# Kernel optimization log

Measured on AMD Instinct MI355X. Metric: run time of the kernel, lower is better.

Reference implementation:

```python
import jax, jax.numpy as jnp
import numpy as np

N = 256  # n_neurons
S = 32   # state_dim
M = 32   # message_dim
E = 32   # edge_dim
B = 64   # batch
N_IN = 16

def setup_inputs() -> dict:
    key = jax.random.key(0)
    ks = jax.random.split(key, 12)
    sc = 0.1
    return {
        "inputs": jax.random.normal(ks[0], (B, N_IN, S), jnp.float32),
        "initial_state": jax.random.normal(ks[1], (N, S), jnp.float32) * sc,
        "edge_matrix": jax.random.normal(ks[2], (N, N, E), jnp.float32) * sc,
        "Wf": jax.random.normal(ks[3], (E, M * S), jnp.float32) * sc,
        "bf": jnp.zeros((M * S,), jnp.float32),
        "Wz": jax.random.normal(ks[4], (M, S), jnp.float32) * sc,
        "Uz": jax.random.normal(ks[5], (S, S), jnp.float32) * sc,
        "bz": jnp.zeros((S,), jnp.float32),
        "Wr": jax.random.normal(ks[6], (M, S), jnp.float32) * sc,
        "Ur": jax.random.normal(ks[7], (S, S), jnp.float32) * sc,
        "br": jnp.zeros((S,), jnp.float32),
        "Wh": jax.random.normal(ks[8], (M, S), jnp.float32) * sc,
        "Uh": jax.random.normal(ks[9], (S, S), jnp.float32) * sc,
        "bh": jnp.zeros((S,), jnp.float32),
        "n_outputs": 16,
    }

def reference(inputs, initial_state, edge_matrix, Wf, bf, Wz, Uz, bz, Wr, Ur, br, Wh, Uh, bh, n_outputs):
    b, n_in, s = inputs.shape
    n = initial_state.shape[0]
    # filter generation: [N,N,E] -> [N,N,M,S]
    filters = (edge_matrix @ Wf + bf).reshape(n, n, M, s)
    # init + scatter inputs into hidden state (neuron i <- inputs[:, i, :])
    h = jnp.tile(initial_state[None], (b, 1, 1)).at[:, :n_in, :].set(inputs)
    # dense edge-filtered message passing: messages[b,j,m] = sum_i filters[i,j,m,s] h[b,i,s]
    messages = jnp.einsum('bis,ijms->bjm', h, filters)
    # GRU update with message as input
    z = jax.nn.sigmoid(messages @ Wz + h @ Uz + bz)
    r = jax.nn.sigmoid(messages @ Wr + h @ Ur + br)
    h_tilde = jnp.tanh(messages @ Wh + (r * h) @ Uh + bh)
    h_new = (1.0 - z) * h + z * h_tilde
    # gather outputs from the last n_outputs neurons (reversed), permute to [n_out, B, S]
    out_idx = n - 1 - jnp.arange(n_outputs)
    outputs = jnp.transpose(h_new[:, out_idx, :], (1, 0, 2))
    return (outputs, h_new)
```

## Files before the change

kernel.cpp:

```cpp
#include <hip/hip_runtime.h>

typedef unsigned short u16;
typedef __attribute__((ext_vector_type(4))) unsigned short u16x4;
typedef __attribute__((ext_vector_type(8))) unsigned short u16x8;
typedef __attribute__((ext_vector_type(4))) float f32x4;
typedef __attribute__((ext_vector_type(16))) float f32x16;


__device__ __forceinline__ u16 f2bf(float x){
  unsigned u = __builtin_bit_cast(unsigned, x);
  u += 0x7FFFu + ((u >> 16) & 1u);
  return (u16)(u >> 16);
}

__device__ __forceinline__ void mfma3232(f32x16& acc, u16x8 a, u16x8 b){
  asm volatile("v_mfma_f32_32x32x16_bf16 %0, %1, %2, %0" : "+v"(acc) : "v"(a), "v"(b));
}
__device__ __forceinline__ void mfma1616(f32x4& acc, u16x8 a, u16x8 b){
  asm volatile("v_mfma_f32_16x16x32_bf16 %0, %1, %2, %0" : "+v"(acc) : "v"(a), "v"(b));
}

__global__ __launch_bounds__(256) void k_ht(const float* __restrict__ inputs,
                                            const float* __restrict__ init,
                                            u16* __restrict__ hT){
  int tid = blockIdx.x*256 + threadIdx.x;
  int base = tid*4;
  int r = base >> 8;
  int i0 = base & 255;
  int b = r >> 5, s = r & 31;
  u16x4 v;
#pragma unroll
  for (int q=0;q<4;++q){
    int i = i0 + q;
    float x = (i < 16) ? inputs[(b*16 + i)*32 + s] : init[i*32 + s];
    v[q] = f2bf(x);
  }
  *(u16x4*)(hT + base) = v;
}

__global__ __launch_bounds__(256) void k_emt(const float* __restrict__ EM, u16* __restrict__ EMT){
  __shared__ float tl[64*65];
  int t = threadIdx.x;
  int i0 = blockIdx.y*64, c0 = blockIdx.x*64;
#pragma unroll
  for (int p=0;p<4;++p){
    int ri = p*16 + (t>>4);
    int c4 = (t&15)*4;
    f32x4 v = *(const f32x4*)(EM + (i0+ri)*8192 + c0 + c4);
#pragma unroll
    for (int q=0;q<4;++q) tl[ri*65 + c4 + q] = v[q];
  }
  __syncthreads();
#pragma unroll
  for (int p=0;p<4;++p){
    int rc = p*16 + (t>>4);
    int i4 = (t&15)*4;
    u16x4 o;
#pragma unroll
    for (int q=0;q<4;++q) o[q] = f2bf(tl[(i4+q)*65 + rc]);
    *(u16x4*)(EMT + (c0+rc)*256 + i0 + i4) = o;
  }
}

__global__ __launch_bounds__(256) void k_wf5(const float* __restrict__ Wf, u16* __restrict__ Wf5){
  int o = (blockIdx.x*256 + threadIdx.x)*4;
  int m = o >> 10, rem = o & 1023, s = rem >> 5, e0 = rem & 31;
  u16x4 v;
#pragma unroll
  for (int q=0;q<4;++q) v[q] = f2bf(Wf[(e0+q)*1024 + m*32 + s]);
  *(u16x4*)(Wf5 + o) = v;
}

__global__ __launch_bounds__(256) void k_bterm(const float* __restrict__ inputs,
                                               const float* __restrict__ init,
                                               const float* __restrict__ bf,
                                               float* __restrict__ bterm){
  __shared__ float red[8][32];
  __shared__ float hsum[32];
  int b = blockIdx.x, t = threadIdx.x;
  int g = t >> 5, s = t & 31;
  float acc = 0.f;
  for (int c=0;c<32;++c){
    int i = c*8 + g;
    acc += (i < 16) ? inputs[(b*16 + i)*32 + s] : init[i*32 + s];
  }
  red[g][s] = acc;
  __syncthreads();
  if (t < 32){
    float v = 0.f;
#pragma unroll
    for (int gg=0;gg<8;++gg) v += red[gg][t];
    hsum[t] = v;
  }
  __syncthreads();
  if (t < 32){
    float v = 0.f;
    for (int s2=0;s2<32;++s2) v += hsum[s2] * bf[t*32 + s2];
    bterm[b*32 + t] = v;
  }
}

__global__ __launch_bounds__(256) void k_gemm(const u16* __restrict__ hT, const u16* __restrict__ EMT,
                                              const u16* __restrict__ Wf5, const float* __restrict__ bterm,
                                              float* __restrict__ msgs){
  __shared__ char smem[81920];
  const int t = threadIdx.x, w = t >> 6, l = t & 63;
  const int rb = blockIdx.x & 31, cb = blockIdx.x >> 5;
  const int r0 = rb*64, c0 = cb*256;
  char* smA = smem;
  char* smB = smem + 16384;

  f32x16 acc[2][2];
#pragma unroll
  for (int a=0;a<2;++a)
#pragma unroll
    for (int bq=0;bq<2;++bq)
#pragma unroll
      for (int q=0;q<16;++q) acc[a][bq][q] = 0.f;

  for (int st=0; st<2; ++st){
    const int kk = st*128;
#pragma unroll
    for (int p=0;p<4;++p){
      int q = p*256 + t;
      int r = q >> 4, k8 = q & 15;
      u16x8 v = *(const u16x8*)(hT + (r0+r)*256 + kk + k8*8);
      *(u16x8*)(smA + r*256 + ((k8*16) ^ ((r&15)<<4))) = v;
    }
#pragma unroll
    for (int p=0;p<16;++p){
      int q = p*256 + t;
      int c = q >> 4, k8 = q & 15;
      u16x8 v = *(const u16x8*)(EMT + (c0+c)*256 + kk + k8*8);
      *(u16x8*)(smB + c*256 + ((k8*16) ^ ((c&15)<<4))) = v;
    }
    __syncthreads();
    const int lane31 = l & 31, kh = (l >> 5)*8;
#pragma unroll
    for (int ks=0; ks<8; ++ks){
      int kbyte = (ks*16 + kh)*2;
      u16x8 a0, a1, b0, b1;
      { int row = lane31;          a0 = *(const u16x8*)(smA + row*256 + (kbyte ^ ((row&15)<<4))); }
      { int row = 32 + lane31;     a1 = *(const u16x8*)(smA + row*256 + (kbyte ^ ((row&15)<<4))); }
      { int col = w*64 + lane31;   b0 = *(const u16x8*)(smB + col*256 + (kbyte ^ ((col&15)<<4))); }
      { int col = w*64 + 32 + lane31; b1 = *(const u16x8*)(smB + col*256 + (kbyte ^ ((col&15)<<4))); }
      mfma3232(acc[0][0], a0, b0);
      mfma3232(acc[0][1], a0, b1);
      mfma3232(acc[1][0], a1, b0);
      mfma3232(acc[1][1], a1, b1);
    }
    __syncthreads();
  }

  u16* T = (u16*)smem;
#pragma unroll
  for (int rbk=0;rbk<2;++rbk)
#pragma unroll
    for (int cbk=0;cbk<2;++cbk){
      int col = w*64 + cbk*32 + (l & 31);
#pragma unroll
      for (int q=0;q<16;++q){
        int row = rbk*32 + (q&3) + 8*(q>>2) + 4*(l>>5);
        T[row*256 + col] = f2bf(acc[rbk][cbk][q]);
      }
    }
  __syncthreads();

  f32x4 eacc0, eacc1;
#pragma unroll
  for (int q=0;q<4;++q){ eacc0[q]=0.f; eacc1[q]=0.f; }
  {
    const int colbj = l & 15;
    const int bloc = colbj >> 3, jloc = colbj & 7;
    const int e0 = (l >> 4)*8;
#pragma unroll
    for (int ss=0; ss<8; ++ss){
      int s = w*8 + ss;
      u16x8 bf_ = *(const u16x8*)((char*)T + (bloc*32 + s)*512 + (jloc*32 + e0)*2);
      u16x8 af0 = *(const u16x8*)(Wf5 + (colbj)*1024 + s*32 + e0);
      u16x8 af1 = *(const u16x8*)(Wf5 + (16 + colbj)*1024 + s*32 + e0);
      mfma1616(eacc0, af0, bf_);
      mfma1616(eacc1, af1, bf_);
    }
  }
  float* red = (float*)(smem + 32768);
  *(f32x4*)(red + ((w*2+0)*64 + l)*4) = eacc0;
  *(f32x4*)(red + ((w*2+1)*64 + l)*4) = eacc1;
  __syncthreads();
  const int b0g = rb*2, j0g = cb*8;
  for (int o = t; o < 512; o += 256){
    int col = o >> 5, m = o & 31;
    int hh = m >> 4, mloc = m & 15;
    int lsrc = col | ((mloc >> 2) << 4);
    int q = mloc & 3;
    float sum = 0.f;
#pragma unroll
    for (int wv=0; wv<4; ++wv) sum += red[((wv*2+hh)*64 + lsrc)*4 + q];
    int bg = b0g + (col >> 3), jg = j0g + (col & 7);
    msgs[(bg*256 + jg)*32 + m] = sum + bterm[bg*32 + m];
  }
}

__global__ __launch_bounds__(256) void k_gru(const float* __restrict__ inputs, const float* __restrict__ init,
    const float* __restrict__ msgs,
    const float* __restrict__ Wz, const float* __restrict__ Uz, const float* __restrict__ bz,
    const float* __restrict__ Wr, const float* __restrict__ Ur, const float* __restrict__ br,
    const float* __restrict__ Wh, const float* __restrict__ Uh, const float* __restrict__ bh,
    float* __restrict__ out){
  __shared__ float L[6*1024 + 96];
  for (int i = threadIdx.x; i < 1024; i += 256){
    L[i] = Wz[i]; L[1024+i] = Uz[i]; L[2048+i] = Wr[i];
    L[3072+i] = Ur[i]; L[4096+i] = Wh[i]; L[5120+i] = Uh[i];
  }
  if (threadIdx.x < 32){
    L[6144+threadIdx.x] = bz[threadIdx.x];
    L[6176+threadIdx.x] = br[threadIdx.x];
    L[6208+threadIdx.x] = bh[threadIdx.x];
  }
  __syncthreads();
  const int t = threadIdx.x, s = t & 31;
  const int rowbase = blockIdx.x*64 + (t>>6)*16 + ((t>>5)&1)*8;
  float mv[8], hv[8], az[8], ar[8];
#pragma unroll
  for (int j=0;j<8;++j){
    int grow = rowbase + j; int b = grow >> 8, n = grow & 255;
    mv[j] = msgs[grow*32 + s];
    hv[j] = (n < 16) ? inputs[(b*16 + n)*32 + s] : init[n*32 + s];
    az[j] = L[6144+s]; ar[j] = L[6176+s];
  }
  for (int k=0;k<32;++k){
    float wz = L[k*32+s], uz = L[1024+k*32+s], wr = L[2048+k*32+s], ur = L[3072+k*32+s];
    int src = (t & 32) | k;
#pragma unroll
    for (int j=0;j<8;++j){
      float mk = __shfl(mv[j], src, 64);
      float hk = __shfl(hv[j], src, 64);
      az[j] += mk*wz + hk*uz;
      ar[j] += mk*wr + hk*ur;
    }
  }
  float zz[8], rh[8], ah[8];
#pragma unroll
  for (int j=0;j<8;++j){
    zz[j] = 1.f/(1.f + __expf(-az[j]));
    float rr = 1.f/(1.f + __expf(-ar[j]));
    rh[j] = rr * hv[j];
    ah[j] = L[6208+s];
  }
  for (int k=0;k<32;++k){
    float wh = L[4096+k*32+s], uh = L[5120+k*32+s];
    int src = (t & 32) | k;
#pragma unroll
    for (int j=0;j<8;++j){
      float mk  = __shfl(mv[j], src, 64);
      float rhk = __shfl(rh[j], src, 64);
      ah[j] += mk*wh + rhk*uh;
    }
  }
#pragma unroll
  for (int j=0;j<8;++j){
    int grow = rowbase + j; int b = grow >> 8, n = grow & 255;
    float ht = tanhf(ah[j]);
    float hn = (1.f - zz[j])*hv[j] + zz[j]*ht;
    out[32768 + grow*32 + s] = hn;
    if (n >= 240) out[(255 - n)*2048 + b*32 + s] = hn;
  }
}

extern "C" void kernel_launch(void* const* d_in, const int* in_sizes, int n_in,
                              void* d_out, int out_size, void* d_ws, size_t ws_size,
                              hipStream_t stream) {
  const float* inputs = (const float*)d_in[0];
  const float* init   = (const float*)d_in[1];
  const float* EM     = (const float*)d_in[2];
  const float* Wf     = (const float*)d_in[3];
  const float* bf     = (const float*)d_in[4];
  const float* Wz     = (const float*)d_in[5];
  const float* Uz     = (const float*)d_in[6];
  const float* bz     = (const float*)d_in[7];
  const float* Wr     = (const float*)d_in[8];
  const float* Ur     = (const float*)d_in[9];
  const float* br     = (const float*)d_in[10];
  const float* Wh     = (const float*)d_in[11];
  const float* Uh     = (const float*)d_in[12];
  const float* bh     = (const float*)d_in[13];
  float* out = (float*)d_out;
  char* ws = (char*)d_ws;

  u16* hT     = (u16*)ws;
  u16* EMT    = (u16*)(ws + (1u<<20));
  u16* Wf5    = (u16*)(ws + (5u<<20));
  float* bterm = (float*)(ws + (5u<<20) + 65536);
  float* msgs  = (float*)(ws + (5u<<20) + 65536 + 8192);

  k_ht   <<<512, 256, 0, stream>>>(inputs, init, hT);
  k_emt  <<<dim3(128,4), 256, 0, stream>>>(EM, EMT);
  k_wf5  <<<32, 256, 0, stream>>>(Wf, Wf5);
  k_bterm<<<64, 256, 0, stream>>>(inputs, init, bf, bterm);
  k_gemm <<<1024, 256, 0, stream>>>(hT, EMT, Wf5, bterm, msgs);
  k_gru  <<<256, 256, 0, stream>>>(inputs, init, msgs, Wz,Uz,bz, Wr,Ur,br, Wh,Uh,bh, out);
}
```

Baseline: 138.0 us.

## Merge prep kernels and fuse GEMM, filter contraction and GRU into one kernel

The four preprocessing kernels become one multi-role launch, and the message GEMM, Wf contraction and GRU update run in a single kernel. The GEMM now uses 128x128 tiles with 16x16 MFMAs, loads tiles straight into LDS with global_load_lds, and asks for 3 blocks per CU via launch bounds. The GRU matmuls move from shuffle-based FP32 FMAs to bf16 MFMAs executed by a single wave per block. This removes launches and the msgs round-trip through global memory, at the cost of lower precision in the GRU and an epilogue where only one wave does the GRU work.

```diff
diff --git a/kernel.cpp b/kernel.cpp
--- a/kernel.cpp
+++ b/kernel.cpp
@@ -4,7 +4,6 @@
 typedef __attribute__((ext_vector_type(4))) unsigned short u16x4;
 typedef __attribute__((ext_vector_type(8))) unsigned short u16x8;
 typedef __attribute__((ext_vector_type(4))) float f32x4;
-typedef __attribute__((ext_vector_type(16))) float f32x16;
 
 
 __device__ __forceinline__ u16 f2bf(float x){
@@ -12,258 +11,262 @@
   u += 0x7FFFu + ((u >> 16) & 1u);
   return (u16)(u >> 16);
 }
-
-__device__ __forceinline__ void mfma3232(f32x16& acc, u16x8 a, u16x8 b){
-  asm volatile("v_mfma_f32_32x32x16_bf16 %0, %1, %2, %0" : "+v"(acc) : "v"(a), "v"(b));
-}
 __device__ __forceinline__ void mfma1616(f32x4& acc, u16x8 a, u16x8 b){
   asm volatile("v_mfma_f32_16x16x32_bf16 %0, %1, %2, %0" : "+v"(acc) : "v"(a), "v"(b));
 }
-
-__global__ __launch_bounds__(256) void k_ht(const float* __restrict__ inputs,
-                                            const float* __restrict__ init,
-                                            u16* __restrict__ hT){
-  int tid = blockIdx.x*256 + threadIdx.x;
-  int base = tid*4;
-  int r = base >> 8;
-  int i0 = base & 255;
-  int b = r >> 5, s = r & 31;
-  u16x4 v;
-#pragma unroll
-  for (int q=0;q<4;++q){
-    int i = i0 + q;
-    float x = (i < 16) ? inputs[(b*16 + i)*32 + s] : init[i*32 + s];
-    v[q] = f2bf(x);
-  }
-  *(u16x4*)(hT + base) = v;
-}
-
-__global__ __launch_bounds__(256) void k_emt(const float* __restrict__ EM, u16* __restrict__ EMT){
+__device__ __forceinline__ void gl16(const void* g, void* l){
+  __builtin_amdgcn_global_load_lds((const __attribute__((address_space(1))) void*)g,
+                                   (__attribute__((address_space(3))) void*)l, 16, 0, 0);
+}
+__device__ __forceinline__ float sigm(float x){ return 1.f/(1.f + __expf(-x)); }
+__device__ __forceinline__ float tanh_f(float x){ return 1.f - 2.f/(1.f + __expf(2.f*x)); }
+
+__global__ __launch_bounds__(256) void k_prep(const float* __restrict__ inputs, const float* __restrict__ init,
+    const float* __restrict__ EM, const float* __restrict__ Wf, const float* __restrict__ bfv,
+    const float* __restrict__ Wz, const float* __restrict__ Uz, const float* __restrict__ Wr,
+    const float* __restrict__ Ur, const float* __restrict__ Wh, const float* __restrict__ Uh,
+    u16* __restrict__ hT, u16* __restrict__ EMT, u16* __restrict__ Wf5,
+    float* __restrict__ bterm, u16* __restrict__ wsT){
   __shared__ float tl[64*65];
-  int t = threadIdx.x;
-  int i0 = blockIdx.y*64, c0 = blockIdx.x*64;
-#pragma unroll
-  for (int p=0;p<4;++p){
-    int ri = p*16 + (t>>4);
-    int c4 = (t&15)*4;
-    f32x4 v = *(const f32x4*)(EM + (i0+ri)*8192 + c0 + c4);
-#pragma unroll
-    for (int q=0;q<4;++q) tl[ri*65 + c4 + q] = v[q];
-  }
+  const int bid = blockIdx.x, t = threadIdx.x;
+  if (bid < 512){
+    int bx = bid & 127, by = bid >> 7;
+    int i0 = by*64, c0 = bx*64;
+#pragma unroll
+    for (int p=0;p<4;++p){
+      int ri = p*16 + (t>>4), c4 = (t&15)*4;
+      f32x4 v = *(const f32x4*)(EM + (i0+ri)*8192 + c0 + c4);
+#pragma unroll
+      for (int q=0;q<4;++q) tl[ri*65 + c4 + q] = v[q];
+    }
+    __syncthreads();
+#pragma unroll
+    for (int p=0;p<4;++p){
+      int rc = p*16 + (t>>4), i4 = (t&15)*4;
+      u16x4 o;
+#pragma unroll
+      for (int q=0;q<4;++q) o[q] = f2bf(tl[(i4+q)*65 + rc]);
+      *(u16x4*)(EMT + (c0+rc)*256 + i0 + i4) = o;
+    }
+  } else if (bid < 1024){
+    int base = ((bid-512)*256 + t)*4;
+    int r = base >> 8, i0 = base & 255;
+    int b = r >> 5, s = r & 31;
+    u16x4 v;
+#pragma unroll
+    for (int q=0;q<4;++q){
+      int i = i0 + q;
+      float x = (i < 16) ? inputs[(b*16 + i)*32 + s] : init[i*32 + s];
+      v[q] = f2bf(x);
+    }
+    *(u16x4*)(hT + base) = v;
+  } else if (bid < 1056){
+    int o = ((bid-1024)*256 + t)*4;
+    int m = o >> 10, rem = o & 1023, s = rem >> 5, e0 = rem & 31;
+    u16x4 v;
+#pragma unroll
+    for (int q=0;q<4;++q) v[q] = f2bf(Wf[(e0+q)*1024 + m*32 + s]);
+    *(u16x4*)(Wf5 + o) = v;
+  } else if (bid < 1120){
+    int b = bid - 1056;
+    float* red = tl;
+    float* hsum = tl + 256;
+    int g = t >> 5, s = t & 31;
+    float acc = 0.f;
+    for (int c=0;c<32;++c){
+      int i = c*8 + g;
+      acc += (i < 16) ? inputs[(b*16 + i)*32 + s] : init[i*32 + s];
+    }
+    red[g*32 + s] = acc;
+    __syncthreads();
+    if (t < 32){
+      float v = 0.f;
+#pragma unroll
+      for (int gg=0;gg<8;++gg) v += red[gg*32 + t];
+      hsum[t] = v;
+    }
+    __syncthreads();
+    if (t < 32){
+      float v = 0.f;
+      for (int s2=0;s2<32;++s2) v += hsum[s2] * bfv[t*32 + s2];
+      bterm[b*32 + t] = v;
+    }
+  } else {
+    const float* Ws[6] = {Wz,Uz,Wr,Ur,Wh,Uh};
+    for (int idx = t; idx < 6144; idx += 256){
+      int g = idx >> 10, r2 = idx & 1023, s = r2 >> 5, k = r2 & 31;
+      wsT[g*1024 + s*32 + k] = f2bf(Ws[g][k*32 + s]);
+    }
+  }
+}
+
+__global__ __launch_bounds__(256, 3) void k_mega(const u16* __restrict__ hT, const u16* __restrict__ EMT,
+    const u16* __restrict__ Wf5, const float* __restrict__ bterm, const u16* __restrict__ wsT,
+    const float* __restrict__ inputs, const float* __restrict__ init,
+    const float* __restrict__ bz, const float* __restrict__ br, const float* __restrict__ bh,
+    float* __restrict__ out){
+  __shared__ char smem[48128];
+  const int t = threadIdx.x, w = t >> 6, l = t & 63;
+  const int rb = blockIdx.x & 15, cb = blockIdx.x >> 4;
+  const int r0 = rb*128, c0 = cb*128;
+  const int wrow = (w >> 1)*64, wcol = (w & 1)*64;
+
+  f32x4 acc[4][4];
+#pragma unroll
+  for (int i=0;i<4;++i)
+#pragma unroll
+    for (int j=0;j<4;++j)
+#pragma unroll
+      for (int q=0;q<4;++q) acc[i][j][q] = 0.f;
+
+  for (int st=0; st<4; ++st){
+    const int kk = st*64;
+#pragma unroll
+    for (int p=0;p<4;++p){
+      int q = p*256 + t, r = q>>3, sl = q&7;
+      gl16(hT + (r0 + r)*256 + kk + ((sl ^ (r&7))*8), smem + q*16);
+    }
+#pragma unroll
+    for (int p=0;p<4;++p){
+      int q = p*256 + t, c = q>>3, sl = q&7;
+      gl16(EMT + (c0 + c)*256 + kk + ((sl ^ (c&7))*8), smem + 16384 + q*16);
+    }
+    __syncthreads();
+#pragma unroll
+    for (int ks=0; ks<2; ++ks){
+      const int kg = ks*4 + (l>>4);
+      u16x8 af[4], bfr[4];
+#pragma unroll
+      for (int mf=0; mf<4; ++mf){
+        int row = wrow + mf*16 + (l&15);
+        af[mf] = *(const u16x8*)(smem + row*128 + ((kg ^ (row&7))<<4));
+      }
+#pragma unroll
+      for (int nf=0; nf<4; ++nf){
+        int col = wcol + nf*16 + (l&15);
+        bfr[nf] = *(const u16x8*)(smem + 16384 + col*128 + ((kg ^ (col&7))<<4));
+      }
+#pragma unroll
+      for (int mf=0; mf<4; ++mf)
+#pragma unroll
+        for (int nf=0; nf<4; ++nf)
+          mfma1616(acc[mf][nf], af[mf], bfr[nf]);
+    }
+    __syncthreads();
+  }
+
+#pragma unroll
+  for (int mf=0;mf<4;++mf)
+#pragma unroll
+    for (int nf=0;nf<4;++nf){
+      int colg = wcol + nf*16 + (l&15);
+#pragma unroll
+      for (int q=0;q<4;++q){
+        int rowg = wrow + mf*16 + (l>>4)*4 + q;
+        *(u16*)(smem + rowg*256 + ((colg*2) ^ ((rowg&7)<<4))) = f2bf(acc[mf][nf][q]);
+      }
+    }
   __syncthreads();
-#pragma unroll
-  for (int p=0;p<4;++p){
-    int rc = p*16 + (t>>4);
-    int i4 = (t&15)*4;
-    u16x4 o;
-#pragma unroll
-    for (int q=0;q<4;++q) o[q] = f2bf(tl[(i4+q)*65 + rc]);
-    *(u16x4*)(EMT + (c0+rc)*256 + i0 + i4) = o;
-  }
-}
-
-__global__ __launch_bounds__(256) void k_wf5(const float* __restrict__ Wf, u16* __restrict__ Wf5){
-  int o = (blockIdx.x*256 + threadIdx.x)*4;
-  int m = o >> 10, rem = o & 1023, s = rem >> 5, e0 = rem & 31;
-  u16x4 v;
-#pragma unroll
-  for (int q=0;q<4;++q) v[q] = f2bf(Wf[(e0+q)*1024 + m*32 + s]);
-  *(u16x4*)(Wf5 + o) = v;
-}
-
-__global__ __launch_bounds__(256) void k_bterm(const float* __restrict__ inputs,
-                                               const float* __restrict__ init,
-                                               const float* __restrict__ bf,
-                                               float* __restrict__ bterm){
-  __shared__ float red[8][32];
-  __shared__ float hsum[32];
-  int b = blockIdx.x, t = threadIdx.x;
-  int g = t >> 5, s = t & 31;
-  float acc = 0.f;
-  for (int c=0;c<32;++c){
-    int i = c*8 + g;
-    acc += (i < 16) ? inputs[(b*16 + i)*32 + s] : init[i*32 + s];
-  }
-  red[g][s] = acc;
-  __syncthreads();
-  if (t < 32){
-    float v = 0.f;
-#pragma unroll
-    for (int gg=0;gg<8;++gg) v += red[gg][t];
-    hsum[t] = v;
-  }
-  __syncthreads();
-  if (t < 32){
-    float v = 0.f;
-    for (int s2=0;s2<32;++s2) v += hsum[s2] * bf[t*32 + s2];
-    bterm[b*32 + t] = v;
-  }
-}
-
-__global__ __launch_bounds__(256) void k_gemm(const u16* __restrict__ hT, const u16* __restrict__ EMT,
-                                              const u16* __restrict__ Wf5, const float* __restrict__ bterm,
-                                              float* __restrict__ msgs){
-  __shared__ char smem[81920];
-  const int t = threadIdx.x, w = t >> 6, l = t & 63;
-  const int rb = blockIdx.x & 31, cb = blockIdx.x >> 5;
-  const int r0 = rb*64, c0 = cb*256;
-  char* smA = smem;
-  char* smB = smem + 16384;
-
-  f32x16 acc[2][2];
-#pragma unroll
-  for (int a=0;a<2;++a)
-#pragma unroll
-    for (int bq=0;bq<2;++bq)
-#pragma unroll
-      for (int q=0;q<16;++q) acc[a][bq][q] = 0.f;
-
-  for (int st=0; st<2; ++st){
-    const int kk = st*128;
-#pragma unroll
-    for (int p=0;p<4;++p){
-      int q = p*256 + t;
-      int r = q >> 4, k8 = q & 15;
-      u16x8 v = *(const u16x8*)(hT + (r0+r)*256 + kk + k8*8);
-      *(u16x8*)(smA + r*256 + ((k8*16) ^ ((r&15)<<4))) = v;
-    }
-#pragma unroll
-    for (int p=0;p<16;++p){
-      int q = p*256 + t;
-      int c = q >> 4, k8 = q & 15;
-      u16x8 v = *(const u16x8*)(EMT + (c0+c)*256 + kk + k8*8);
-      *(u16x8*)(smB + c*256 + ((k8*16) ^ ((c&15)<<4))) = v;
-    }
-    __syncthreads();
-    const int lane31 = l & 31, kh = (l >> 5)*8;
-#pragma unroll
-    for (int ks=0; ks<8; ++ks){
-      int kbyte = (ks*16 + kh)*2;
-      u16x8 a0, a1, b0, b1;
-      { int row = lane31;          a0 = *(const u16x8*)(smA + row*256 + (kbyte ^ ((row&15)<<4))); }
-      { int row = 32 + lane31;     a1 = *(const u16x8*)(smA + row*256 + (kbyte ^ ((row&15)<<4))); }
-      { int col = w*64 + lane31;   b0 = *(const u16x8*)(smB + col*256 + (kbyte ^ ((col&15)<<4))); }
-      { int col = w*64 + 32 + lane31; b1 = *(const u16x8*)(smB + col*256 + (kbyte ^ ((col&15)<<4))); }
-      mfma3232(acc[0][0], a0, b0);
-      mfma3232(acc[0][1], a0, b1);
-      mfma3232(acc[1][0], a1, b0);
-      mfma3232(acc[1][1], a1, b1);
-    }
-    __syncthreads();
-  }
-
-  u16* T = (u16*)smem;
-#pragma unroll
-  for (int rbk=0;rbk<2;++rbk)
-#pragma unroll
-    for (int cbk=0;cbk<2;++cbk){
-      int col = w*64 + cbk*32 + (l & 31);
-#pragma unroll
-      for (int q=0;q<16;++q){
-        int row = rbk*32 + (q&3) + 8*(q>>2) + 4*(l>>5);
-        T[row*256 + col] = f2bf(acc[rbk][cbk][q]);
-      }
-    }
-  __syncthreads();
-
-  f32x4 eacc0, eacc1;
-#pragma unroll
-  for (int q=0;q<4;++q){ eacc0[q]=0.f; eacc1[q]=0.f; }
+
+  f32x4 ea0, ea1;
+#pragma unroll
+  for (int q=0;q<4;++q){ ea0[q]=0.f; ea1[q]=0.f; }
   {
     const int colbj = l & 15;
-    const int bloc = colbj >> 3, jloc = colbj & 7;
-    const int e0 = (l >> 4)*8;
+    const int bloc = colbj >> 2, jloc = colbj & 3;
+    const int eg = (l >> 4)*8;
 #pragma unroll
     for (int ss=0; ss<8; ++ss){
       int s = w*8 + ss;
-      u16x8 bf_ = *(const u16x8*)((char*)T + (bloc*32 + s)*512 + (jloc*32 + e0)*2);
-      u16x8 af0 = *(const u16x8*)(Wf5 + (colbj)*1024 + s*32 + e0);
-      u16x8 af1 = *(const u16x8*)(Wf5 + (16 + colbj)*1024 + s*32 + e0);
-      mfma1616(eacc0, af0, bf_);
-      mfma1616(eacc1, af1, bf_);
+      int row = bloc*32 + s;
+      u16x8 bfr = *(const u16x8*)(smem + row*256 + ((jloc*64 + eg*2) ^ ((row&7)<<4)));
+      u16x8 af0 = *(const u16x8*)(Wf5 + colbj*1024 + s*32 + eg);
+      u16x8 af1 = *(const u16x8*)(Wf5 + (16+colbj)*1024 + s*32 + eg);
+      mfma1616(ea0, af0, bfr);
+      mfma1616(ea1, af1, bfr);
     }
   }
   float* red = (float*)(smem + 32768);
-  *(f32x4*)(red + ((w*2+0)*64 + l)*4) = eacc0;
-  *(f32x4*)(red + ((w*2+1)*64 + l)*4) = eacc1;
+  *(f32x4*)(red + ((w*2+0)*64 + l)*4) = ea0;
+  *(f32x4*)(red + ((w*2+1)*64 + l)*4) = ea1;
   __syncthreads();
-  const int b0g = rb*2, j0g = cb*8;
+
+  float* Lmsg = (float*)(smem + 40960);
+  u16*   Lmsgb = (u16*)(smem + 43008);
+  float* Lh   = (float*)(smem + 44032);
+  u16*   Lhb  = (u16*)(smem + 46080);
+  u16*   Lrh  = (u16*)(smem + 47104);
   for (int o = t; o < 512; o += 256){
-    int col = o >> 5, m = o & 31;
+    int row = o >> 5, m = o & 31;
     int hh = m >> 4, mloc = m & 15;
-    int lsrc = col | ((mloc >> 2) << 4);
+    int lsrc = row | ((mloc >> 2) << 4);
     int q = mloc & 3;
     float sum = 0.f;
 #pragma unroll
     for (int wv=0; wv<4; ++wv) sum += red[((wv*2+hh)*64 + lsrc)*4 + q];
-    int bg = b0g + (col >> 3), jg = j0g + (col & 7);
-    msgs[(bg*256 + jg)*32 + m] = sum + bterm[bg*32 + m];
-  }
-}
-
-__global__ __launch_bounds__(256) void k_gru(const float* __restrict__ inputs, const float* __restrict__ init,
-    const float* __restrict__ msgs,
-    const float* __restrict__ Wz, const float* __restrict__ Uz, const float* __restrict__ bz,
-    const float* __restrict__ Wr, const float* __restrict__ Ur, const float* __restrict__ br,
-    const float* __restrict__ Wh, const float* __restrict__ Uh, const float* __restrict__ bh,
-    float* __restrict__ out){
-  __shared__ float L[6*1024 + 96];
-  for (int i = threadIdx.x; i < 1024; i += 256){
-    L[i] = Wz[i]; L[1024+i] = Uz[i]; L[2048+i] = Wr[i];
-    L[3072+i] = Ur[i]; L[4096+i] = Wh[i]; L[5120+i] = Uh[i];
-  }
-  if (threadIdx.x < 32){
-    L[6144+threadIdx.x] = bz[threadIdx.x];
-    L[6176+threadIdx.x] = br[threadIdx.x];
-    L[6208+threadIdx.x] = bh[threadIdx.x];
+    int bg = rb*4 + (row>>2), jg = cb*4 + (row&3);
+    float mval = sum + bterm[bg*32 + m];
+    Lmsg[row*32+m] = mval; Lmsgb[row*32+m] = f2bf(mval);
+    float hval = (jg < 16) ? inputs[(bg*16 + jg)*32 + m] : init[jg*32 + m];
+    Lh[row*32+m] = hval; Lhb[row*32+m] = f2bf(hval);
   }
   __syncthreads();
-  const int t = threadIdx.x, s = t & 31;
-  const int rowbase = blockIdx.x*64 + (t>>6)*16 + ((t>>5)&1)*8;
-  float mv[8], hv[8], az[8], ar[8];
-#pragma unroll
-  for (int j=0;j<8;++j){
-    int grow = rowbase + j; int b = grow >> 8, n = grow & 255;
-    mv[j] = msgs[grow*32 + s];
-    hv[j] = (n < 16) ? inputs[(b*16 + n)*32 + s] : init[n*32 + s];
-    az[j] = L[6144+s]; ar[j] = L[6176+s];
-  }
-  for (int k=0;k<32;++k){
-    float wz = L[k*32+s], uz = L[1024+k*32+s], wr = L[2048+k*32+s], ur = L[3072+k*32+s];
-    int src = (t & 32) | k;
-#pragma unroll
-    for (int j=0;j<8;++j){
-      float mk = __shfl(mv[j], src, 64);
-      float hk = __shfl(hv[j], src, 64);
-      az[j] += mk*wz + hk*uz;
-      ar[j] += mk*wr + hk*ur;
-    }
-  }
-  float zz[8], rh[8], ah[8];
-#pragma unroll
-  for (int j=0;j<8;++j){
-    zz[j] = 1.f/(1.f + __expf(-az[j]));
-    float rr = 1.f/(1.f + __expf(-ar[j]));
-    rh[j] = rr * hv[j];
-    ah[j] = L[6208+s];
-  }
-  for (int k=0;k<32;++k){
-    float wh = L[4096+k*32+s], uh = L[5120+k*32+s];
-    int src = (t & 32) | k;
-#pragma unroll
-    for (int j=0;j<8;++j){
-      float mk  = __shfl(mv[j], src, 64);
-      float rhk = __shfl(rh[j], src, 64);
-      ah[j] += mk*wh + rhk*uh;
-    }
-  }
-#pragma unroll
-  for (int j=0;j<8;++j){
-    int grow = rowbase + j; int b = grow >> 8, n = grow & 255;
-    float ht = tanhf(ah[j]);
-    float hn = (1.f - zz[j])*hv[j] + zz[j]*ht;
-    out[32768 + grow*32 + s] = hn;
-    if (n >= 240) out[(255 - n)*2048 + b*32 + s] = hn;
+
+  if (w == 0){
+    const int rloc = l & 15;
+    const int kg8 = (l >> 4)*8;
+    u16x8 am = *(const u16x8*)(Lmsgb + rloc*32 + kg8);
+    u16x8 ah = *(const u16x8*)(Lhb   + rloc*32 + kg8);
+    u16x8 wz0 = *(const u16x8*)(wsT + 0*1024 + rloc*32 + kg8);
+    u16x8 wz1 = *(const u16x8*)(wsT + 0*1024 + (16+rloc)*32 + kg8);
+    u16x8 uz0 = *(const u16x8*)(wsT + 1*1024 + rloc*32 + kg8);
+    u16x8 uz1 = *(const u16x8*)(wsT + 1*1024 + (16+rloc)*32 + kg8);
+    u16x8 wr0 = *(const u16x8*)(wsT + 2*1024 + rloc*32 + kg8);
+    u16x8 wr1 = *(const u16x8*)(wsT + 2*1024 + (16+rloc)*32 + kg8);
+    u16x8 ur0 = *(const u16x8*)(wsT + 3*1024 + rloc*32 + kg8);
+    u16x8 ur1 = *(const u16x8*)(wsT + 3*1024 + (16+rloc)*32 + kg8);
+    u16x8 wh0 = *(const u16x8*)(wsT + 4*1024 + rloc*32 + kg8);
+    u16x8 wh1 = *(const u16x8*)(wsT + 4*1024 + (16+rloc)*32 + kg8);
+    u16x8 uh0 = *(const u16x8*)(wsT + 5*1024 + rloc*32 + kg8);
+    u16x8 uh1 = *(const u16x8*)(wsT + 5*1024 + (16+rloc)*32 + kg8);
+    f32x4 zp0,zp1,rp0,rp1,hp0,hp1;
+#pragma unroll
+    for (int q=0;q<4;++q){ zp0[q]=0;zp1[q]=0;rp0[q]=0;rp1[q]=0;hp0[q]=0;hp1[q]=0; }
+    mfma1616(zp0, am, wz0); mfma1616(zp0, ah, uz0);
+    mfma1616(zp1, am, wz1); mfma1616(zp1, ah, uz1);
+    mfma1616(rp0, am, wr0); mfma1616(rp0, ah, ur0);
+    mfma1616(rp1, am, wr1); mfma1616(rp1, ah, ur1);
+    mfma1616(hp0, am, wh0);
+    mfma1616(hp1, am, wh1);
+    const int crow = (l>>4)*4, cs = l & 15;
+    float bz0 = bz[cs], bz1 = bz[16+cs], br0 = br[cs], br1 = br[16+cs];
+    f32x4 z0,z1;
+#pragma unroll
+    for (int q=0;q<4;++q){
+      z0[q] = sigm(zp0[q]+bz0); z1[q] = sigm(zp1[q]+bz1);
+      float r0 = sigm(rp0[q]+br0), r1 = sigm(rp1[q]+br1);
+      Lrh[(crow+q)*32 + cs]    = f2bf(r0 * Lh[(crow+q)*32 + cs]);
+      Lrh[(crow+q)*32 + 16+cs] = f2bf(r1 * Lh[(crow+q)*32 + 16+cs]);
+    }
+    u16x8 arh = *(const u16x8*)(Lrh + rloc*32 + kg8);
+    mfma1616(hp0, arh, uh0);
+    mfma1616(hp1, arh, uh1);
+    float bh0 = bh[cs], bh1 = bh[16+cs];
+#pragma unroll
+    for (int q=0;q<4;++q){
+      int rw = crow + q;
+      float ht0 = tanh_f(hp0[q]+bh0), ht1 = tanh_f(hp1[q]+bh1);
+      float h0 = Lh[rw*32+cs], h1 = Lh[rw*32+16+cs];
+      float hn0 = (1.f - z0[q])*h0 + z0[q]*ht0;
+      float hn1 = (1.f - z1[q])*h1 + z1[q]*ht1;
+      int bg = rb*4 + (rw>>2), jg = cb*4 + (rw&3);
+      int base = 32768 + (bg*256 + jg)*32;
+      out[base + cs] = hn0; out[base + 16 + cs] = hn1;
+      if (jg >= 240){
+        int ob = (255-jg)*2048 + bg*32;
+        out[ob + cs] = hn0; out[ob + 16 + cs] = hn1;
+      }
+    }
   }
 }
 
@@ -274,7 +277,7 @@
   const float* init   = (const float*)d_in[1];
   const float* EM     = (const float*)d_in[2];
   const float* Wf     = (const float*)d_in[3];
-  const float* bf     = (const float*)d_in[4];
+  const float* bfv    = (const float*)d_in[4];
   const float* Wz     = (const float*)d_in[5];
   const float* Uz     = (const float*)d_in[6];
   const float* bz     = (const float*)d_in[7];
@@ -287,16 +290,13 @@
   float* out = (float*)d_out;
   char* ws = (char*)d_ws;
 
-  u16* hT     = (u16*)ws;
-  u16* EMT    = (u16*)(ws + (1u<<20));
-  u16* Wf5    = (u16*)(ws + (5u<<20));
+  u16* hT      = (u16*)ws;
+  u16* EMT     = (u16*)(ws + (1u<<20));
+  u16* Wf5     = (u16*)(ws + (5u<<20));
   float* bterm = (float*)(ws + (5u<<20) + 65536);
-  float* msgs  = (float*)(ws + (5u<<20) + 65536 + 8192);
-
-  k_ht   <<<512, 256, 0, stream>>>(inputs, init, hT);
-  k_emt  <<<dim3(128,4), 256, 0, stream>>>(EM, EMT);
-  k_wf5  <<<32, 256, 0, stream>>>(Wf, Wf5);
-  k_bterm<<<64, 256, 0, stream>>>(inputs, init, bf, bterm);
-  k_gemm <<<1024, 256, 0, stream>>>(hT, EMT, Wf5, bterm, msgs);
-  k_gru  <<<256, 256, 0, stream>>>(inputs, init, msgs, Wz,Uz,bz, Wr,Ur,br, Wh,Uh,bh, out);
-}
+  u16* wsT     = (u16*)(ws + (5u<<20) + 65536 + 8192);
+
+  k_prep<<<1121, 256, 0, stream>>>(inputs, init, EM, Wf, bfv, Wz, Uz, Wr, Ur, Wh, Uh,
+                                   hT, EMT, Wf5, bterm, wsT);
+  k_mega<<<1024, 256, 0, stream>>>(hT, EMT, Wf5, bterm, wsT, inputs, init, bz, br, bh, out);
+}
```

Measured after the change: 121.1 us. -12.3%, faster.
